# Performance work log

Measured on AMD Instinct MI355X. Metric: run time of the kernel, lower is better.

## Reference

```python
import jax, jax.numpy as jnp
import numpy as np

DN = ('NCHW', 'OIHW', 'NCHW')

def _conv(x, w, stride, pad, groups=1):
    return jax.lax.conv_general_dilated(x, w, (stride, stride), pad,
                                        feature_group_count=groups,
                                        dimension_numbers=DN)

def _bn(x, s, b):
    # eval-mode BatchNorm folded to per-channel affine
    return x * s[:, None, None] + b[:, None, None]

def _gelu(x):
    return jax.nn.gelu(x, approximate=False)  # torch nn.GELU default = exact erf

def _region_dw(x, dw_w, s1, b1, pw_w, s2, b2, g):
    # Vectorized RegionLayerDW: split [B,C,H,W] into g*g tiles, apply per-tile
    # depthwise3x3 -> BN -> GELU -> 1x1 -> BN -> +residual, reassemble.
    B, C, H, W = x.shape
    th, tw = H // g, W // g
    t = x.reshape(B, C, g, th, g, tw).transpose(2, 4, 0, 1, 3, 5)
    t = t.reshape(g * g, B, C, th, tw)  # [G,B,C,th,tw]
    def tile(xt, w, ts1, tb1, pw, ts2, tb2):
        h = _conv(xt, w, 1, ((1, 1), (1, 1)), groups=C)  # depthwise 3x3
        h = _gelu(_bn(h, ts1, tb1))
        h = jnp.einsum('bchw,oc->bohw', h, pw)  # 1x1 conv
        return _bn(h, ts2, tb2) + xt
    y = jax.vmap(tile)(t, dw_w, s1, b1, pw_w, s2, b2)
    y = y.reshape(g, g, B, C, th, tw).transpose(2, 3, 0, 4, 1, 5)
    return y.reshape(B, C, H, W)

def _forward(x, r1_w, r1_s, r1_b, r1_dw, r1_s1, r1_b1, r1_pw, r1_s2, r1_b2,
             r2_w, r2_s, r2_b, r2_dw, r2_s1, r2_b1, r2_pw, r2_s2, r2_b2,
             h1_w1, h1_s1, h1_b1, h1_w2, h1_s2, h1_b2, h1_w3, h1_s3, h1_b3,
             h2_w1, h2_s1, h2_b1, h2_w2, h2_s2, h2_b2,
             h3_w, h3_s, h3_b):
    B = x.shape[0]
    # region1: 5x5 conv 3->24, BN, GELU, RegionLayerDW grid 7x7; then outer GELU
    r1 = _gelu(_bn(_conv(x, r1_w, 1, ((2, 2), (2, 2))), r1_s, r1_b))
    r1 = _region_dw(r1, r1_dw, r1_s1, r1_b1, r1_pw, r1_s2, r1_b2, 7)
    region1 = _gelu(r1)
    # region2: 3x3 conv 24->48, BN, GELU, RegionLayerDW grid 4x4; outer GELU
    r2 = _gelu(_bn(_conv(region1, r2_w, 1, ((1, 1), (1, 1))), r2_s, r2_b))
    r2 = _region_dw(r2, r2_dw, r2_s1, r2_b1, r2_pw, r2_s2, r2_b2, 4)
    region2 = _gelu(r2)
    # hMLP branch1: 3 -> 48(k4s4) -> 48(k2s2) -> 256(k2s2)
    h = _gelu(_bn(_conv(x, h1_w1, 4, 'VALID'), h1_s1, h1_b1))
    h = _gelu(_bn(_conv(h, h1_w2, 2, 'VALID'), h1_s2, h1_b2))
    branch1 = _bn(_conv(h, h1_w3, 2, 'VALID'), h1_s3, h1_b3)
    # hMLP branch2: 24 -> 48(k4s4) -> 256(k4s4)
    g2 = _gelu(_bn(_conv(region1, h2_w1, 4, 'VALID'), h2_s1, h2_b1))
    branch2 = _bn(_conv(g2, h2_w2, 4, 'VALID'), h2_s2, h2_b2)
    # hMLP branch3: 48 -> 256(k16s16)
    branch3 = _bn(_conv(region2, h3_w, 16, 'VALID'), h3_s, h3_b)
    out = jnp.concatenate((branch1, branch2, branch3), axis=1)  # [B,768,14,14]
    return jnp.transpose(out.reshape(B, out.shape[1], -1), (0, 2, 1))  # [B,196,768]


def setup_inputs() -> dict:
    key = jax.random.key(0)
    ks = [key]
    def nk():
        ks[0], k = jax.random.split(ks[0])
        return k
    def rn(shape, scale=0.05):
        return jax.random.normal(nk(), shape, jnp.float32) * scale
    def sc(shape):
        return 1.0 + rn(shape)
    B = 16
    d = {}
    d['x'] = rn((B, 3, 224, 224), 1.0)
    d['r1_w'] = rn((24, 3, 5, 5)); d['r1_s'] = sc((24,)); d['r1_b'] = rn((24,))
    d['r1_dw'] = rn((49, 24, 1, 3, 3)); d['r1_s1'] = sc((49, 24)); d['r1_b1'] = rn((49, 24))
    d['r1_pw'] = rn((49, 24, 24)); d['r1_s2'] = sc((49, 24)); d['r1_b2'] = rn((49, 24))
    d['r2_w'] = rn((48, 24, 3, 3)); d['r2_s'] = sc((48,)); d['r2_b'] = rn((48,))
    d['r2_dw'] = rn((16, 48, 1, 3, 3)); d['r2_s1'] = sc((16, 48)); d['r2_b1'] = rn((16, 48))
    d['r2_pw'] = rn((16, 48, 48)); d['r2_s2'] = sc((16, 48)); d['r2_b2'] = rn((16, 48))
    d['h1_w1'] = rn((48, 3, 4, 4)); d['h1_s1'] = sc((48,)); d['h1_b1'] = rn((48,))
    d['h1_w2'] = rn((48, 48, 2, 2)); d['h1_s2'] = sc((48,)); d['h1_b2'] = rn((48,))
    d['h1_w3'] = rn((256, 48, 2, 2)); d['h1_s3'] = sc((256,)); d['h1_b3'] = rn((256,))
    d['h2_w1'] = rn((48, 24, 4, 4)); d['h2_s1'] = sc((48,)); d['h2_b1'] = rn((48,))
    d['h2_w2'] = rn((256, 48, 4, 4)); d['h2_s2'] = sc((256,)); d['h2_b2'] = rn((256,))
    d['h3_w'] = rn((256, 48, 16, 16)); d['h3_s'] = sc((256,)); d['h3_b'] = rn((256,))
    return d


def reference(x, r1_w, r1_s, r1_b, r1_dw, r1_s1, r1_b1, r1_pw, r1_s2, r1_b2,
              r2_w, r2_s, r2_b, r2_dw, r2_s1, r2_b1, r2_pw, r2_s2, r2_b2,
              h1_w1, h1_s1, h1_b1, h1_w2, h1_s2, h1_b2, h1_w3, h1_s3, h1_b3,
              h2_w1, h2_s1, h2_b1, h2_w2, h2_s2, h2_b2,
              h3_w, h3_s, h3_b):
    return _forward(x, r1_w, r1_s, r1_b, r1_dw, r1_s1, r1_b1, r1_pw, r1_s2, r1_b2,
                    r2_w, r2_s, r2_b, r2_dw, r2_s1, r2_b1, r2_pw, r2_s2, r2_b2,
                    h1_w1, h1_s1, h1_b1, h1_w2, h1_s2, h1_b2, h1_w3, h1_s3, h1_b3,
                    h2_w1, h2_s1, h2_b1, h2_w2, h2_s2, h2_b2,
                    h3_w, h3_s, h3_b)
```

## Files before the change

kernel.cpp:

```cpp
#include <hip/hip_runtime.h>
#include <hip/hip_bf16.h>
#include <math.h>

typedef __attribute__((ext_vector_type(8))) short short8;
typedef __attribute__((ext_vector_type(4))) float f32x4;

__device__ __forceinline__ float gelu_f(float x) {
  float ax = fabsf(x);
  float z = ax * 0.70710678118654752f;
  float t = __builtin_amdgcn_rcpf(1.0f + 0.3275911f * z);
  float p = t * (0.254829592f +
           t * (-0.284496736f +
           t * (1.421413741f +
           t * (-1.453152027f + t * 1.061405429f))));
  float e = __expf(-z * z);
  float erf_abs = 1.0f - p * e;
  return 0.5f * x + 0.5f * ax * erf_abs;
}

template<bool TBL, bool GELU, bool TOOUT>
__global__ __launch_bounds__(256) void convgemm_k(
    const float* __restrict__ in, const float* __restrict__ w,
    const float* __restrict__ bns, const float* __restrict__ bnb,
    float* __restrict__ out,
    int Cin, int H, int W, int ks, int stride, int pad, int ls,
    int OH, int OW, int N, int K, int ch0) {
  __shared__ __align__(16) float sA[16][64];
  __shared__ __align__(16) float sB[16][64];
  __shared__ int sTbl[256];
  const int tid = threadIdx.x;
  if (TBL) {
    int kk2 = ks * ks;
    for (int k = tid; k < K; k += 256) {
      int ic = k / kk2, r = k - ic * kk2;
      sTbl[k] = (ic << 16) | ((r / ks) << 8) | (r % ks);
    }
  }
  const int m0 = blockIdx.x * 64, n0 = blockIdx.y * 64;
  const int mm = tid >> 2, kq = tid & 3;
  const int OHW = OH * OW, HW = H * W;
  int m = m0 + mm;
  int bI = m / OHW; int r = m - bI * OHW;
  int oh = r / OW;  int ow = r - oh * OW;
  const int ihBase = oh * stride - pad, iwBase = ow * stride - pad;
  const int inBase = bI * Cin * HW;
  const int tm = tid & 15, tn = tid >> 4;
  float acc[4][4] = {};
  for (int k0 = 0; k0 < K; k0 += 16) {
    __syncthreads();
#pragma unroll
    for (int i = 0; i < 4; ++i) {
      int kk = kq * 4 + i, k = k0 + kk;
      float v = 0.0f;
      if (k < K) {
        int ic, dy, dx;
        if (TBL) {
          int tv = sTbl[k]; ic = tv >> 16; dy = (tv >> 8) & 255; dx = tv & 255;
        } else {
          ic = k >> (2 * ls);
          int r2 = k & ((1 << (2 * ls)) - 1);
          dy = r2 >> ls; dx = r2 & ((1 << ls) - 1);
        }
        int ih = ihBase + dy, iw = iwBase + dx;
        if (ih >= 0 && ih < H && iw >= 0 && iw < W)
          v = in[inBase + ic * HW + ih * W + iw];
      }
      sA[kk][mm] = v;
    }
#pragma unroll
    for (int i = 0; i < 4; ++i) {
      int kk = kq * 4 + i, k = k0 + kk;
      int n = n0 + mm;
      float v = 0.0f;
      if (n < N && k < K) v = w[n * K + k];
      sB[kk][mm] = v;
    }
    __syncthreads();
#pragma unroll
    for (int kk = 0; kk < 16; ++kk) {
      float4 a4 = *(const float4*)&sA[kk][tm * 4];
      float4 b4 = *(const float4*)&sB[kk][tn * 4];
      acc[0][0] += a4.x * b4.x; acc[0][1] += a4.x * b4.y;
      acc[0][2] += a4.x * b4.z; acc[0][3] += a4.x * b4.w;
      acc[1][0] += a4.y * b4.x; acc[1][1] += a4.y * b4.y;
      acc[1][2] += a4.y * b4.z; acc[1][3] += a4.y * b4.w;
      acc[2][0] += a4.z * b4.x; acc[2][1] += a4.z * b4.y;
      acc[2][2] += a4.z * b4.z; acc[2][3] += a4.z * b4.w;
      acc[3][0] += a4.w * b4.x; acc[3][1] += a4.w * b4.y;
      acc[3][2] += a4.w * b4.z; acc[3][3] += a4.w * b4.w;
    }
  }
#pragma unroll
  for (int i = 0; i < 4; ++i) {
    int mI = m0 + tm * 4 + i;
    int bO = mI / OHW; int rr = mI - bO * OHW;
#pragma unroll
    for (int j = 0; j < 4; ++j) {
      int n = n0 + tn * 4 + j;
      if (n < N) {
        float v = acc[i][j] * bns[n] + bnb[n];
        if (GELU) v = gelu_f(v);
        if (TOOUT) {
          out[(bO * OHW + rr) * 768 + ch0 + n] = v;
        } else {
          int oh2 = rr / OW, ow2 = rr - oh2 * OW;
          out[((bO * N + n) * OH + oh2) * OW + ow2] = v;
        }
      }
    }
  }
}

template<int CIN, int KS, int STRIDE, int PAD, int NN, int KP, bool GELU,
         int OUTMODE, int NVALID = NN>
__global__ __launch_bounds__(256) void nhwc_conv_mfma(
    const __hip_bfloat16* __restrict__ in, const __hip_bfloat16* __restrict__ wb,
    const float* __restrict__ bns, const float* __restrict__ bnb,
    float* __restrict__ out, int Hin, int Win, int OW, int OHW) {
  constexpr int K = KS * KS * CIN;
  constexpr int LROW = KP + 8;
  __shared__ __align__(16) __hip_bfloat16 sA[64][LROW];
  __shared__ __align__(16) __hip_bfloat16 sB[NN][LROW];
  const int tid = threadIdx.x;
  const float4 f4z = make_float4(0.f, 0.f, 0.f, 0.f);
  if constexpr (CIN == 4) {
    const int m = tid & 63, tg = tid >> 6;
    const int mg = blockIdx.x * 64 + m;
    const int bI = mg / OHW; int pix = mg - bI * OHW;
    const int oh = pix / OW, ow = pix - oh * OW;
    for (int dy = tg; dy < KS; dy += 4) {
      const int ih = oh * STRIDE - PAD + dy;
      __hip_bfloat16* dst = &sA[m][dy * KS * 4];
#pragma unroll
      for (int j = 0; j < KS; ++j) {
        int iw = ow * STRIDE - PAD + j;
        uint2 v = make_uint2(0u, 0u);
        if (ih >= 0 && ih < Hin && iw >= 0 && iw < Win)
          v = *(const uint2*)(in + (((size_t)bI * Hin + ih) * Win + iw) * 4);
        *(uint2*)(dst + j * 4) = v;
      }
    }
    if (tg == 3) {
      for (int c = K; c < KP; c += 4) *(uint2*)&sA[m][c] = make_uint2(0u, 0u);
    }
  } else {
    const int m = tid & 63, dy = tid >> 6;
    const int mg = blockIdx.x * 64 + m;
    const int bI = mg / OHW; int pix = mg - bI * OHW;
    const int oh = pix / OW, ow = pix - oh * OW;
    if (dy < KS) {
      const int ih = oh * STRIDE - PAD + dy;
      __hip_bfloat16* dst = &sA[m][dy * KS * CIN];
      if (ih < 0 || ih >= Hin) {
#pragma unroll
        for (int i = 0; i < KS * CIN / 8; ++i) ((float4*)dst)[i] = f4z;
      } else {
        const __hip_bfloat16* srow = in + ((size_t)bI * Hin + ih) * Win * CIN;
#pragma unroll
        for (int j = 0; j < KS; ++j) {
          int iw = ow * STRIDE - PAD + j;
          if (PAD > 0 && (iw < 0 || iw >= Win)) {
#pragma unroll
            for (int i = 0; i < CIN / 8; ++i) ((float4*)(dst + j * CIN))[i] = f4z;
          } else {
            const float4* s4 = (const float4*)(srow + (size_t)iw * CIN);
#pragma unroll
            for (int i = 0; i < CIN / 8; ++i) ((float4*)(dst + j * CIN))[i] = s4[i];
          }
        }
      }
    } else if (K < KP) {
#pragma unroll
      for (int c = K; c < KP + 8; c += 8) *(float4*)&sA[m][c] = f4z;
    }
  }
  {
    constexpr int NV = NN * KP / 8;
    const float4* w4 = (const float4*)wb;
    for (int i = tid; i < NV; i += 256) {
      int n = i / (KP / 8), c = i - n * (KP / 8);
      *(float4*)&sB[n][c * 8] = w4[i];
    }
  }
  __syncthreads();
  constexpr int NT = NN / 16;
  const int wave = tid >> 6, lane = tid & 63;
  const int fm = lane & 15, quad = lane >> 4;
  const int wm = wave * 16;
  f32x4 acc[NT] = {};
#pragma unroll
  for (int ks = 0; ks < KP / 32; ++ks) {
    short8 a = *(const short8*)&sA[wm + fm][ks * 32 + quad * 8];
#pragma unroll
    for (int j = 0; j < NT; ++j) {
      short8 b = *(const short8*)&sB[j * 16 + fm][ks * 32 + quad * 8];
      acc[j] = __builtin_amdgcn_mfma_f32_16x16x32_bf16(a, b, acc[j], 0, 0, 0);
    }
  }
  const int mg0 = blockIdx.x * 64 + wm + quad * 4;
  const int bI = mg0 / OHW, pix = mg0 - bI * OHW;
#pragma unroll
  for (int j = 0; j < NT; ++j) {
    int n = j * 16 + fm;
    if (n >= NVALID) continue;
    float s = bns[n], bb = bnb[n];
    float v[4];
#pragma unroll
    for (int e = 0; e < 4; ++e) {
      v[e] = acc[j][e] * s + bb;
      if (GELU) v[e] = gelu_f(v[e]);
    }
    if (OUTMODE == 0) {
      float4 v4 = make_float4(v[0], v[1], v[2], v[3]);
      *(float4*)&out[((size_t)(bI * NVALID + n)) * OHW + pix] = v4;
    } else {
      __hip_bfloat16* ob = (__hip_bfloat16*)out;
#pragma unroll
      for (int e = 0; e < 4; ++e)
        ob[((size_t)(bI * OHW + pix + e)) * NVALID + n] = (__hip_bfloat16)v[e];
    }
  }
}

__global__ __launch_bounds__(256, 4) void region2_mfma(
    const __hip_bfloat16* __restrict__ in, const float* __restrict__ dww,
    const float* __restrict__ s1v, const float* __restrict__ b1v,
    const __hip_bfloat16* __restrict__ pwb,
    const float* __restrict__ s2v, const float* __restrict__ b2v,
    __hip_bfloat16* __restrict__ out) {
  __shared__ __align__(16) __hip_bfloat16 sIn[10][10][56];
  __shared__ __align__(16) __hip_bfloat16 sH[64][64];
  __shared__ __align__(16) __hip_bfloat16 sW[48][64];
  __shared__ float sDW[48][9];
  __shared__ float sS1[48], sB1[48], sS2[48], sB2[48];
  const int t = blockIdx.x, sb = blockIdx.y, b = blockIdx.z;
  const int gy = t >> 2, gx = t & 3;
  const int py0 = (sb / 7) * 8, px0 = (sb % 7) * 8;
  const int Y0 = gy * 56, X0 = gx * 56;
  const int tid = threadIdx.x;
  for (int i = tid; i < 48 * 8; i += 256) {
    int n = i >> 3, g = i & 7;
    float4 v = *(const float4*)&pwb[(size_t)(t * 48 + n) * 64 + g * 8];
    *(float4*)&sW[n][((g ^ (n & 7)) * 8)] = v;
  }
  for (int i = tid; i < 432; i += 256) ((float*)sDW)[i] = dww[t * 432 + i];
  if (tid < 48) {
    sS1[tid] = s1v[t * 48 + tid]; sB1[tid] = b1v[t * 48 + tid];
    sS2[tid] = s2v[t * 48 + tid]; sB2[tid] = b2v[t * 48 + tid];
  }
  for (int i = tid; i < 600; i += 256) {
    int px = i / 6, grp = i - px * 6;
    int r = px / 10, c = px - r * 10;
    int ly = py0 + r - 1, lx = px0 + c - 1;
    uint4 v = make_uint4(0u, 0u, 0u, 0u);
    if (ly >= 0 && ly < 56 && lx >= 0 && lx < 56)
      v = *(const uint4*)(in + (((size_t)b * 224 + Y0 + ly) * 224 + X0 + lx) * 48 +
                          grp * 8);
    *(uint4*)&sIn[r][c][grp * 8] = v;
  }
  __syncthreads();
  if (tid < 192) {
    const int cg = tid >> 4;
    const int rem = tid & 15;
    const int col = rem >> 1;
    const int rh = rem & 1;
    const int ch0 = cg * 4;
    float wv[4][9], s14[4], b14[4];
#pragma unroll
    for (int c4 = 0; c4 < 4; ++c4) {
#pragma unroll
      for (int q = 0; q < 9; ++q) wv[c4][q] = sDW[ch0 + c4][q];
      s14[c4] = sS1[ch0 + c4]; b14[c4] = sB1[ch0 + c4];
    }
    float win[3][12];
#pragma unroll
    for (int rr = 0; rr < 6; ++rr) {
      int r = rh * 4 + rr;
      float* wr = win[rr % 3];
#pragma unroll
      for (int cc = 0; cc < 3; ++cc) {
        uint2 u = *(const uint2*)&sIn[r][col + cc][ch0];
        wr[cc * 4 + 0] = __uint_as_float(u.x << 16);
        wr[cc * 4 + 1] = __uint_as_float(u.x & 0xffff0000u);
        wr[cc * 4 + 2] = __uint_as_float(u.y << 16);
        wr[cc * 4 + 3] = __uint_as_float(u.y & 0xffff0000u);
      }
      if (rr >= 2) {
        const float* ra = win[(rr - 2) % 3];
        const float* rb = win[(rr - 1) % 3];
        const float* rc = win[rr % 3];
        int px = (rh * 4 + rr - 2) * 8 + col;
        __hip_bfloat16 hv[4];
#pragma unroll
        for (int c4 = 0; c4 < 4; ++c4) {
          float a = ra[c4] * wv[c4][0] + ra[4 + c4] * wv[c4][1] + ra[8 + c4] * wv[c4][2]
                  + rb[c4] * wv[c4][3] + rb[4 + c4] * wv[c4][4] + rb[8 + c4] * wv[c4][5]
                  + rc[c4] * wv[c4][6] + rc[4 + c4] * wv[c4][7] + rc[8 + c4] * wv[c4][8];
          hv[c4] = (__hip_bfloat16)gelu_f(a * s14[c4] + b14[c4]);
        }
        *(uint2*)&sH[px][((cg >> 1) ^ (px & 7)) * 8 + (cg & 1) * 4] = *(uint2*)hv;
      }
    }
  } else {
    for (int i = tid - 192; i < 128; i += 64) {
      int px = i >> 1, g = 6 + (i & 1);
      *(float4*)&sH[px][(g ^ (px & 7)) * 8] = make_float4(0.f, 0.f, 0.f, 0.f);
    }
  }
  __syncthreads();
  const int wave = tid >> 6, lane = tid & 63;
  const int fm = lane & 15, quad = lane >> 4;
  const int px = wave * 16 + fm, pxk = px & 7;
  f32x4 acc[3] = {};
#pragma unroll
  for (int ks = 0; ks < 2; ++ks) {
    short8 hb = *(const short8*)&sH[px][((ks * 4 + quad) ^ pxk) * 8];
#pragma unroll
    for (int m = 0; m < 3; ++m) {
      int wr = m * 16 + fm;
      short8 wa = *(const short8*)&sW[wr][((ks * 4 + quad) ^ (wr & 7)) * 8];
      acc[m] = __builtin_amdgcn_mfma_f32_16x16x32_bf16(wa, hb, acc[m], 0, 0, 0);
    }
  }
  const int row = px >> 3, col = px & 7;
  __hip_bfloat16* obase =
      out + (((size_t)b * 224 + Y0 + py0 + row) * 224 + X0 + px0 + col) * 48;
#pragma unroll
  for (int m = 0; m < 3; ++m) {
    int ch0m = m * 16 + quad * 4;
    uint2 ru = *(const uint2*)&sIn[row + 1][col + 1][ch0m];
    float res[4];
    res[0] = __uint_as_float(ru.x << 16);
    res[1] = __uint_as_float(ru.x & 0xffff0000u);
    res[2] = __uint_as_float(ru.y << 16);
    res[3] = __uint_as_float(ru.y & 0xffff0000u);
    __hip_bfloat16 vb[4];
#pragma unroll
    for (int e = 0; e < 4; ++e) {
      int ch = ch0m + e;
      float v = acc[m][e] * sS2[ch] + sB2[ch] + res[e];
      vb[e] = (__hip_bfloat16)gelu_f(v);
    }
    *(uint2*)&obase[ch0m] = *(uint2*)vb;
  }
}

__global__ __launch_bounds__(256, 4) void region1_mfma(
    const __hip_bfloat16* __restrict__ in, const float* __restrict__ dww,
    const float* __restrict__ s1v, const float* __restrict__ b1v,
    const __hip_bfloat16* __restrict__ pwb,
    const float* __restrict__ s2v, const float* __restrict__ b2v,
    __hip_bfloat16* __restrict__ out) {
  __shared__ __align__(16) __hip_bfloat16 sIn[10][10][24];
  __shared__ __align__(16) __hip_bfloat16 sH[64][32];
  __shared__ __align__(16) __hip_bfloat16 sW[32][32];
  __shared__ float sDW[24][9];
  __shared__ float sS1[24], sB1[24], sS2[24], sB2[24];
  const int t = blockIdx.x, sb = blockIdx.y, b = blockIdx.z;
  const int gy = t / 7, gx = t % 7;
  const int py0 = (sb >> 2) * 8, px0 = (sb & 3) * 8;
  const int Y0 = gy * 32, X0 = gx * 32;
  const int tid = threadIdx.x;
  for (int i = tid; i < 128; i += 256) {
    int n = i >> 2, g = i & 3;
    float4 v = make_float4(0.f, 0.f, 0.f, 0.f);
    if (n < 24) v = *(const float4*)&pwb[(size_t)(t * 24 + n) * 32 + g * 8];
    *(float4*)&sW[n][(g ^ (n & 3)) * 8] = v;
  }
  for (int i = tid; i < 216; i += 256) ((float*)sDW)[i] = dww[t * 216 + i];
  if (tid < 24) {
    sS1[tid] = s1v[t * 24 + tid]; sB1[tid] = b1v[t * 24 + tid];
    sS2[tid] = s2v[t * 24 + tid]; sB2[tid] = b2v[t * 24 + tid];
  }
  for (int i = tid; i < 300; i += 256) {
    int px = i / 3, grp = i - px * 3;
    int r = px / 10, c = px - r * 10;
    int ly = py0 + r - 1, lx = px0 + c - 1;
    uint4 v = make_uint4(0u, 0u, 0u, 0u);
    if (ly >= 0 && ly < 32 && lx >= 0 && lx < 32)
      v = *(const uint4*)(in + (((size_t)b * 224 + Y0 + ly) * 224 + X0 + lx) * 24 +
                          grp * 8);
    *(uint4*)&sIn[r][c][grp * 8] = v;
  }
  __syncthreads();
  if (tid < 192) {
    const int cg = tid >> 5;
    const int rem = tid & 31;
    const int col = rem >> 2;
    const int rq = rem & 3;
    const int ch0 = cg * 4;
    float wv[4][9], s14[4], b14[4];
#pragma unroll
    for (int c4 = 0; c4 < 4; ++c4) {
#pragma unroll
      for (int q = 0; q < 9; ++q) wv[c4][q] = sDW[ch0 + c4][q];
      s14[c4] = sS1[ch0 + c4]; b14[c4] = sB1[ch0 + c4];
    }
    float win[3][12];
#pragma unroll
    for (int rr = 0; rr < 4; ++rr) {
      int r = rq * 2 + rr;
      float* wr = win[rr % 3];
#pragma unroll
      for (int cc = 0; cc < 3; ++cc) {
        uint2 u = *(const uint2*)&sIn[r][col + cc][ch0];
        wr[cc * 4 + 0] = __uint_as_float(u.x << 16);
        wr[cc * 4 + 1] = __uint_as_float(u.x & 0xffff0000u);
        wr[cc * 4 + 2] = __uint_as_float(u.y << 16);
        wr[cc * 4 + 3] = __uint_as_float(u.y & 0xffff0000u);
      }
      if (rr >= 2) {
        const float* ra = win[(rr - 2) % 3];
        const float* rb = win[(rr - 1) % 3];
        const float* rc = win[rr % 3];
        int px = (rq * 2 + rr - 2) * 8 + col;
        __hip_bfloat16 hv[4];
#pragma unroll
        for (int c4 = 0; c4 < 4; ++c4) {
          float a = ra[c4] * wv[c4][0] + ra[4 + c4] * wv[c4][1] + ra[8 + c4] * wv[c4][2]
                  + rb[c4] * wv[c4][3] + rb[4 + c4] * wv[c4][4] + rb[8 + c4] * wv[c4][5]
                  + rc[c4] * wv[c4][6] + rc[4 + c4] * wv[c4][7] + rc[8 + c4] * wv[c4][8];
          hv[c4] = (__hip_bfloat16)gelu_f(a * s14[c4] + b14[c4]);
        }
        *(uint2*)&sH[px][((cg >> 1) ^ (px & 3)) * 8 + (cg & 1) * 4] = *(uint2*)hv;
      }
    }
  } else {
    int px = tid - 192;
    *(float4*)&sH[px][(3 ^ (px & 3)) * 8] = make_float4(0.f, 0.f, 0.f, 0.f);
  }
  __syncthreads();
  const int wave = tid >> 6, lane = tid & 63;
  const int fm = lane & 15, quad = lane >> 4;
  const int px = wave * 16 + fm;
  short8 hb = *(const short8*)&sH[px][(quad ^ (px & 3)) * 8];
  f32x4 acc[2] = {};
#pragma unroll
  for (int m = 0; m < 2; ++m) {
    int wr = m * 16 + fm;
    short8 wa = *(const short8*)&sW[wr][(quad ^ (wr & 3)) * 8];
    acc[m] = __builtin_amdgcn_mfma_f32_16x16x32_bf16(wa, hb, acc[m], 0, 0, 0);
  }
  const int row = px >> 3, col = px & 7;
  __hip_bfloat16* obase =
      out + (((size_t)b * 224 + Y0 + py0 + row) * 224 + X0 + px0 + col) * 24;
#pragma unroll
  for (int m = 0; m < 2; ++m) {
    int ch0m = m * 16 + quad * 4;
    if (ch0m < 24) {
      uint2 ru = *(const uint2*)&sIn[row + 1][col + 1][ch0m];
      float res[4];
      res[0] = __uint_as_float(ru.x << 16);
      res[1] = __uint_as_float(ru.x & 0xffff0000u);
      res[2] = __uint_as_float(ru.y << 16);
      res[3] = __uint_as_float(ru.y & 0xffff0000u);
      __hip_bfloat16 vb[4];
#pragma unroll
      for (int e = 0; e < 4; ++e) {
        int ch = ch0m + e;
        float v = acc[m][e] * sS2[ch] + sB2[ch] + res[e];
        vb[e] = (__hip_bfloat16)gelu_f(v);
      }
      *(uint2*)&obase[ch0m] = *(uint2*)vb;
    }
  }
}

template<int PS, int IMGW, int KTOT, int KSL, bool ATOMIC>
__global__ __launch_bounds__(256) void patch_gemm_mfma(
    const __hip_bfloat16* __restrict__ A, const __hip_bfloat16* __restrict__ Wb,
    const float* __restrict__ scale, const float* __restrict__ bias,
    float* __restrict__ out, int M, int ch0) {
  constexpr int RUN = PS * 48;
  __shared__ __align__(16) __hip_bfloat16 sA[64][64];
  __shared__ __align__(16) __hip_bfloat16 sB[64][64];
  const int tid = threadIdx.x;
  const int m0 = blockIdx.x * 64, n0 = blockIdx.y * 64;
  const int kBase = blockIdx.z * KSL;
  const int mi = tid >> 2, seg = tid & 3;
  int m = m0 + mi; int mc = (m < M) ? m : (M - 1);
  int bI = mc / 196; int r = mc - bI * 196;
  int oh = r / 14, ow = r - oh * 14;
  const __hip_bfloat16* Abase =
      A + (((size_t)bI * IMGW + oh * PS) * IMGW + ow * PS) * 48;
  const __hip_bfloat16* Wrow = Wb + (size_t)(n0 + mi) * KTOT;
  const int wave = tid >> 6, lane = tid & 63;
  const int wm = (wave & 1) * 32, wn = (wave >> 1) * 32;
  const int fm = lane & 15, quad = lane >> 4;
  const int sw = fm & 7;
  f32x4 acc[2][2] = {};
  for (int k0 = kBase; k0 < kBase + KSL; k0 += 64) {
    int dy = k0 / RUN, rem = k0 - dy * RUN;
    __syncthreads();
    {
      const __hip_bfloat16* p = Abase + (size_t)dy * IMGW * 48 + rem + seg * 16;
      float4 v0 = *(const float4*)p;
      float4 v1 = *(const float4*)(p + 8);
      int key = mi & 7;
      *(float4*)&sA[mi][((seg * 2) ^ key) * 8] = v0;
      *(float4*)&sA[mi][((seg * 2 + 1) ^ key) * 8] = v1;
      const __hip_bfloat16* q = Wrow + k0 + seg * 16;
      float4 w0 = *(const float4*)q;
      float4 w1 = *(const float4*)(q + 8);
      *(float4*)&sB[mi][((seg * 2) ^ key) * 8] = w0;
      *(float4*)&sB[mi][((seg * 2 + 1) ^ key) * 8] = w1;
    }
    __syncthreads();
#pragma unroll
    for (int ks = 0; ks < 2; ++ks) {
      int cg = (ks * 4 + quad) ^ sw;
#pragma unroll
      for (int i = 0; i < 2; ++i) {
        short8 a = *(const short8*)&sA[wm + i * 16 + fm][cg * 8];
#pragma unroll
        for (int j = 0; j < 2; ++j) {
          short8 b = *(const short8*)&sB[wn + j * 16 + fm][cg * 8];
          acc[i][j] = __builtin_amdgcn_mfma_f32_16x16x32_bf16(a, b, acc[i][j], 0, 0, 0);
        }
      }
    }
  }
#pragma unroll
  for (int i = 0; i < 2; ++i) {
#pragma unroll
    for (int j = 0; j < 2; ++j) {
      int gn = n0 + wn + j * 16 + fm;
      float sc = scale[gn];
#pragma unroll
      for (int e = 0; e < 4; ++e) {
        int gm = m0 + wm + i * 16 + quad * 4 + e;
        if (gm < M) {
          if (ATOMIC)
            atomicAdd(&out[(size_t)gm * 768 + ch0 + gn], acc[i][j][e] * sc);
          else
            out[(size_t)gm * 768 + ch0 + gn] = acc[i][j][e] * sc + bias[gn];
        }
      }
    }
  }
}

__global__ void init_b3(float* __restrict__ out, const float* __restrict__ bias) {
  int i = blockIdx.x * 256 + threadIdx.x;
  if (i < 16 * 196 * 256) {
    int n = i & 255, bp = i >> 8;
    out[bp * 768 + 512 + n] = bias[n];
  }
}

__global__ void reorder_w_k(const float* __restrict__ w, __hip_bfloat16* __restrict__ o,
                            int N, int Cin, int ks, int KP) {
  int i = blockIdx.x * 256 + threadIdx.x;
  if (i >= N * KP) return;
  int n = i / KP, k = i - n * KP;
  float v = 0.f;
  int K = ks * ks * Cin;
  if (k < K) {
    int dy = k / (ks * Cin); int r = k - dy * ks * Cin;
    int dx = r / Cin, ic = r - dx * Cin;
    v = w[((n * Cin + ic) * ks + dy) * ks + dx];
  }
  o[i] = (__hip_bfloat16)v;
}

__global__ void reorder_w4(const float* __restrict__ w, __hip_bfloat16* __restrict__ o,
                           int Nout, int Nreal, int Cp, int Cr, int ks, int KP) {
  int i = blockIdx.x * 256 + threadIdx.x;
  if (i >= Nout * KP) return;
  int n = i / KP, k = i - n * KP;
  float v = 0.f;
  if (n < Nreal && k < ks * ks * Cp) {
    int dy = k / (ks * Cp); int r = k - dy * ks * Cp;
    int dx = r / Cp, ic = r - dx * Cp;
    if (ic < Cr) v = w[((n * Cr + ic) * ks + dy) * ks + dx];
  }
  o[i] = (__hip_bfloat16)v;
}

__global__ void rw_pw(const float* __restrict__ pw, __hip_bfloat16* __restrict__ o) {
  int i = blockIdx.x * 256 + threadIdx.x;
  if (i >= 16 * 48 * 64) return;
  int t = i / 3072, r = i - t * 3072;
  int n = r >> 6, k = r & 63;
  float v = (k < 48) ? pw[(t * 48 + n) * 48 + k] : 0.f;
  o[i] = (__hip_bfloat16)v;
}

__global__ void rw_pw1(const float* __restrict__ pw, __hip_bfloat16* __restrict__ o) {
  int i = blockIdx.x * 256 + threadIdx.x;
  if (i >= 49 * 24 * 32) return;
  int t = i / 768, r = i - t * 768;
  int n = r >> 5, k = r & 31;
  float v = (k < 24) ? pw[(t * 24 + n) * 24 + k] : 0.f;
  o[i] = (__hip_bfloat16)v;
}

__global__ void xcvt(const float* __restrict__ x, __hip_bfloat16* __restrict__ o) {
  int i = blockIdx.x * 256 + threadIdx.x;
  if (i >= 802816) return;
  int b = i / 50176, p = i - b * 50176;
  const float* src = x + (size_t)b * 150528 + p;
  __hip_bfloat16 v[4];
  v[0] = (__hip_bfloat16)src[0];
  v[1] = (__hip_bfloat16)src[50176];
  v[2] = (__hip_bfloat16)src[100352];
  v[3] = (__hip_bfloat16)0.0f;
  *(uint2*)&o[(size_t)i * 4] = *(uint2*)v;
}

extern "C" void kernel_launch(void* const* d_in, const int* in_sizes, int n_in,
                              void* d_out, int out_size, void* d_ws, size_t ws_size,
                              hipStream_t stream) {
  const float* x     = (const float*)d_in[0];
  const float* r1_w  = (const float*)d_in[1];
  const float* r1_s  = (const float*)d_in[2];
  const float* r1_b  = (const float*)d_in[3];
  const float* r1_dw = (const float*)d_in[4];
  const float* r1_s1 = (const float*)d_in[5];
  const float* r1_b1 = (const float*)d_in[6];
  const float* r1_pw = (const float*)d_in[7];
  const float* r1_s2 = (const float*)d_in[8];
  const float* r1_b2 = (const float*)d_in[9];
  const float* r2_w  = (const float*)d_in[10];
  const float* r2_s  = (const float*)d_in[11];
  const float* r2_b  = (const float*)d_in[12];
  const float* r2_dw = (const float*)d_in[13];
  const float* r2_s1 = (const float*)d_in[14];
  const float* r2_b1 = (const float*)d_in[15];
  const float* r2_pw = (const float*)d_in[16];
  const float* r2_s2 = (const float*)d_in[17];
  const float* r2_b2 = (const float*)d_in[18];
  const float* h1_w1 = (const float*)d_in[19];
  const float* h1_s1 = (const float*)d_in[20];
  const float* h1_b1 = (const float*)d_in[21];
  const float* h1_w2 = (const float*)d_in[22];
  const float* h1_s2 = (const float*)d_in[23];
  const float* h1_b2 = (const float*)d_in[24];
  const float* h1_w3 = (const float*)d_in[25];
  const float* h1_s3 = (const float*)d_in[26];
  const float* h1_b3 = (const float*)d_in[27];
  const float* h2_w1 = (const float*)d_in[28];
  const float* h2_s1 = (const float*)d_in[29];
  const float* h2_b1 = (const float*)d_in[30];
  const float* h2_w2 = (const float*)d_in[31];
  const float* h2_s2 = (const float*)d_in[32];
  const float* h2_b2 = (const float*)d_in[33];
  const float* h3_w  = (const float*)d_in[34];
  const float* h3_s  = (const float*)d_in[35];
  const float* h3_b  = (const float*)d_in[36];
  float* out = (float*)d_out;

  float* F = (float*)d_ws;
  __hip_bfloat16* R1b   = (__hip_bfloat16*)F;
  __hip_bfloat16* C5b   = (__hip_bfloat16*)(F + 9633792);
  __hip_bfloat16* T1b   = (__hip_bfloat16*)(F + 9633792);
  __hip_bfloat16* T2b   = (__hip_bfloat16*)(F + 28901376);
  __hip_bfloat16* h3wb  = (__hip_bfloat16*)(F + 48168960);
  __hip_bfloat16* r2wb  = (__hip_bfloat16*)(F + 49741824);
  __hip_bfloat16* h2w1b = (__hip_bfloat16*)(F + 49747200);
  __hip_bfloat16* pw2wb = (__hip_bfloat16*)(F + 49756416);
  __hip_bfloat16* r1wb  = (__hip_bfloat16*)(F + 49780992);
  __hip_bfloat16* h2w2b = (__hip_bfloat16*)(F + 49783040);
  __hip_bfloat16* xb    = (__hip_bfloat16*)(F + 49881344);
  __hip_bfloat16* S1b   = (__hip_bfloat16*)(F + 51486976);
  float* S1             = F + 52691200;
  float* S2             = F + 55099648;
  __hip_bfloat16* pw1wb = (__hip_bfloat16*)(F + 55701760);

  dim3 blk(256);

  xcvt<<<dim3(3136), blk, 0, stream>>>(x, xb);
  reorder_w_k<<<dim3(12288), blk, 0, stream>>>(h3_w, h3wb, 256, 48, 16, 12288);
  reorder_w_k<<<dim3(42), blk, 0, stream>>>(r2_w, r2wb, 48, 24, 3, 224);
  reorder_w_k<<<dim3(72), blk, 0, stream>>>(h2_w1, h2w1b, 48, 24, 4, 384);
  reorder_w_k<<<dim3(768), blk, 0, stream>>>(h2_w2, h2w2b, 256, 48, 4, 768);
  reorder_w4<<<dim3(16), blk, 0, stream>>>(r1_w, r1wb, 32, 24, 4, 3, 5, 128);
  rw_pw<<<dim3(192), blk, 0, stream>>>(r2_pw, pw2wb);
  rw_pw1<<<dim3(147), blk, 0, stream>>>(r1_pw, pw1wb);

  nhwc_conv_mfma<4, 5, 1, 2, 32, 128, true, 1, 24><<<dim3(12544), blk, 0, stream>>>(
      xb, r1wb, r1_s, r1_b, (float*)C5b, 224, 224, 224, 50176);
  region1_mfma<<<dim3(49, 16, 16), blk, 0, stream>>>(
      C5b, r1_dw, r1_s1, r1_b1, pw1wb, r1_s2, r1_b2, R1b);
  nhwc_conv_mfma<24, 4, 4, 0, 48, 384, true, 1><<<dim3(784), blk, 0, stream>>>(
      R1b, h2w1b, h2_s1, h2_b1, (float*)S1b, 224, 224, 56, 3136);
  patch_gemm_mfma<4, 56, 768, 768, false><<<dim3(49, 4, 1), blk, 0, stream>>>(
      S1b, h2w2b, h2_s2, h2_b2, out, 3136, 256);
  convgemm_k<false, true, false><<<dim3(784, 1), blk, 0, stream>>>(
      x, h1_w1, h1_s1, h1_b1, S1, 3, 224, 224, 4, 4, 0, 2, 56, 56, 48, 48, 0);
  convgemm_k<false, true, false><<<dim3(196, 1), blk, 0, stream>>>(
      S1, h1_w2, h1_s2, h1_b2, S2, 48, 56, 56, 2, 2, 0, 1, 28, 28, 48, 192, 0);
  convgemm_k<false, false, true><<<dim3(49, 4), blk, 0, stream>>>(
      S2, h1_w3, h1_s3, h1_b3, out, 48, 28, 28, 2, 2, 0, 1, 14, 14, 256, 192, 0);
  init_b3<<<dim3(3136), blk, 0, stream>>>(out, h3_b);
  nhwc_conv_mfma<24, 3, 1, 1, 48, 224, true, 1><<<dim3(12544), blk, 0, stream>>>(
      R1b, r2wb, r2_s, r2_b, (float*)T1b, 224, 224, 224, 50176);
  region2_mfma<<<dim3(16, 49, 16), blk, 0, stream>>>(
      T1b, r2_dw, r2_s1, r2_b1, pw2wb, r2_s2, r2_b2, T2b);
  patch_gemm_mfma<16, 224, 12288, 1536, true><<<dim3(49, 4, 8), blk, 0, stream>>>(
      T2b, h3wb, h3_s, h3_b, out, 3136, 512);
  (void)in_sizes; (void)n_in; (void)out_size; (void)ws_size;
}
```

Baseline: 573.1 us.

## Swap MFMA operands in NHWC conv to vectorize bf16 stores and drop weight LDS staging

The NHWC implicit-GEMM conv kernel now puts weights in the MFMA A operand and pixels in B, so each lane's four accumulators hold four consecutive channels of one pixel. That lets the epilogue pack four bf16 values into a single 8-byte store instead of four scattered 2-byte stores. Weights are read straight from global memory (L1/L2-cached) rather than staged in shared memory, which removes the LDS fill loop and its footprint. The unused fp32 NCHW output mode is removed. The cost is repeated global weight loads inside the inner loop, which may stall on memory latency.

```diff
diff --git a/kernel.cpp b/kernel.cpp
--- a/kernel.cpp
+++ b/kernel.cpp
@@ -112,15 +112,14 @@
 }
 
 template<int CIN, int KS, int STRIDE, int PAD, int NN, int KP, bool GELU,
-         int OUTMODE, int NVALID = NN>
+         int NVALID = NN>
 __global__ __launch_bounds__(256) void nhwc_conv_mfma(
     const __hip_bfloat16* __restrict__ in, const __hip_bfloat16* __restrict__ wb,
     const float* __restrict__ bns, const float* __restrict__ bnb,
-    float* __restrict__ out, int Hin, int Win, int OW, int OHW) {
+    __hip_bfloat16* __restrict__ out, int Hin, int Win, int OW, int OHW) {
   constexpr int K = KS * KS * CIN;
   constexpr int LROW = KP + 8;
   __shared__ __align__(16) __hip_bfloat16 sA[64][LROW];
-  __shared__ __align__(16) __hip_bfloat16 sB[NN][LROW];
   const int tid = threadIdx.x;
   const float4 f4z = make_float4(0.f, 0.f, 0.f, 0.f);
   if constexpr (CIN == 4) {
@@ -174,50 +173,37 @@
       for (int c = K; c < KP + 8; c += 8) *(float4*)&sA[m][c] = f4z;
     }
   }
-  {
-    constexpr int NV = NN * KP / 8;
-    const float4* w4 = (const float4*)wb;
-    for (int i = tid; i < NV; i += 256) {
-      int n = i / (KP / 8), c = i - n * (KP / 8);
-      *(float4*)&sB[n][c * 8] = w4[i];
-    }
-  }
   __syncthreads();
   constexpr int NT = NN / 16;
   const int wave = tid >> 6, lane = tid & 63;
   const int fm = lane & 15, quad = lane >> 4;
-  const int wm = wave * 16;
+  const int p = wave * 16 + fm;
   f32x4 acc[NT] = {};
 #pragma unroll
   for (int ks = 0; ks < KP / 32; ++ks) {
-    short8 a = *(const short8*)&sA[wm + fm][ks * 32 + quad * 8];
-#pragma unroll
-    for (int j = 0; j < NT; ++j) {
-      short8 b = *(const short8*)&sB[j * 16 + fm][ks * 32 + quad * 8];
-      acc[j] = __builtin_amdgcn_mfma_f32_16x16x32_bf16(a, b, acc[j], 0, 0, 0);
-    }
-  }
-  const int mg0 = blockIdx.x * 64 + wm + quad * 4;
+    short8 hb = *(const short8*)&sA[p][ks * 32 + quad * 8];
+#pragma unroll
+    for (int m = 0; m < NT; ++m) {
+      short8 wa = *(const short8*)(wb + (size_t)(m * 16 + fm) * KP + ks * 32 + quad * 8);
+      acc[m] = __builtin_amdgcn_mfma_f32_16x16x32_bf16(wa, hb, acc[m], 0, 0, 0);
+    }
+  }
+  const int mg0 = blockIdx.x * 64 + p;
   const int bI = mg0 / OHW, pix = mg0 - bI * OHW;
-#pragma unroll
-  for (int j = 0; j < NT; ++j) {
-    int n = j * 16 + fm;
-    if (n >= NVALID) continue;
-    float s = bns[n], bb = bnb[n];
-    float v[4];
-#pragma unroll
-    for (int e = 0; e < 4; ++e) {
-      v[e] = acc[j][e] * s + bb;
-      if (GELU) v[e] = gelu_f(v[e]);
-    }
-    if (OUTMODE == 0) {
-      float4 v4 = make_float4(v[0], v[1], v[2], v[3]);
-      *(float4*)&out[((size_t)(bI * NVALID + n)) * OHW + pix] = v4;
-    } else {
-      __hip_bfloat16* ob = (__hip_bfloat16*)out;
-#pragma unroll
-      for (int e = 0; e < 4; ++e)
-        ob[((size_t)(bI * OHW + pix + e)) * NVALID + n] = (__hip_bfloat16)v[e];
+  __hip_bfloat16* obase = out + ((size_t)bI * OHW + pix) * NVALID;
+#pragma unroll
+  for (int m = 0; m < NT; ++m) {
+    int ch0m = m * 16 + quad * 4;
+    if (ch0m < NVALID) {
+      __hip_bfloat16 vb[4];
+#pragma unroll
+      for (int e = 0; e < 4; ++e) {
+        int ch = ch0m + e;
+        float v = acc[m][e] * bns[ch] + bnb[ch];
+        if (GELU) v = gelu_f(v);
+        vb[e] = (__hip_bfloat16)v;
+      }
+      *(uint2*)&obase[ch0m] = *(uint2*)vb;
     }
   }
 }
@@ -678,12 +664,12 @@
   rw_pw<<<dim3(192), blk, 0, stream>>>(r2_pw, pw2wb);
   rw_pw1<<<dim3(147), blk, 0, stream>>>(r1_pw, pw1wb);
 
-  nhwc_conv_mfma<4, 5, 1, 2, 32, 128, true, 1, 24><<<dim3(12544), blk, 0, stream>>>(
-      xb, r1wb, r1_s, r1_b, (float*)C5b, 224, 224, 224, 50176);
+  nhwc_conv_mfma<4, 5, 1, 2, 32, 128, true, 24><<<dim3(12544), blk, 0, stream>>>(
+      xb, r1wb, r1_s, r1_b, C5b, 224, 224, 224, 50176);
   region1_mfma<<<dim3(49, 16, 16), blk, 0, stream>>>(
       C5b, r1_dw, r1_s1, r1_b1, pw1wb, r1_s2, r1_b2, R1b);
-  nhwc_conv_mfma<24, 4, 4, 0, 48, 384, true, 1><<<dim3(784), blk, 0, stream>>>(
-      R1b, h2w1b, h2_s1, h2_b1, (float*)S1b, 224, 224, 56, 3136);
+  nhwc_conv_mfma<24, 4, 4, 0, 48, 384, true><<<dim3(784), blk, 0, stream>>>(
+      R1b, h2w1b, h2_s1, h2_b1, S1b, 224, 224, 56, 3136);
   patch_gemm_mfma<4, 56, 768, 768, false><<<dim3(49, 4, 1), blk, 0, stream>>>(
       S1b, h2w2b, h2_s2, h2_b2, out, 3136, 256);
   convgemm_k<false, true, false><<<dim3(784, 1), blk, 0, stream>>>(
@@ -693,8 +679,8 @@
   convgemm_k<false, false, true><<<dim3(49, 4), blk, 0, stream>>>(
       S2, h1_w3, h1_s3, h1_b3, out, 48, 28, 28, 2, 2, 0, 1, 14, 14, 256, 192, 0);
   init_b3<<<dim3(3136), blk, 0, stream>>>(out, h3_b);
-  nhwc_conv_mfma<24, 3, 1, 1, 48, 224, true, 1><<<dim3(12544), blk, 0, stream>>>(
-      R1b, r2wb, r2_s, r2_b, (float*)T1b, 224, 224, 224, 50176);
+  nhwc_conv_mfma<24, 3, 1, 1, 48, 224, true><<<dim3(12544), blk, 0, stream>>>(
+      R1b, r2wb, r2_s, r2_b, T1b, 224, 224, 224, 50176);
   region2_mfma<<<dim3(16, 49, 16), blk, 0, stream>>>(
       T1b, r2_dw, r2_s1, r2_b1, pw2wb, r2_s2, r2_b2, T2b);
   patch_gemm_mfma<16, 224, 12288, 1536, true><<<dim3(49, 4, 8), blk, 0, stream>>>(
```

Measured after the change: 629.0 us. 1.1x slower.
